# Kernel optimization log

Hardware: AMD Instinct MI355X
Metric: run time of the kernel (lower is better)

## Reference

```python
import jax, jax.numpy as jnp
import numpy as np

B, T, S, F, D, M = 8, 8192, 8192, 64, 64, 128
EPS = 1e-9


def _draw_omega(n_omega, d_feature, rng):
    # Stacked orthogonal blocks scaled by sqrt(d_feature), as in the TF module.
    n_blocks = (n_omega + d_feature - 1) // d_feature + 1
    blocks = []
    for _ in range(n_blocks):
        g = rng.standard_normal((d_feature, d_feature)).astype(np.float32)
        q, _ = np.linalg.qr(g)
        blocks.append(q * np.sqrt(float(d_feature)))
    return jnp.asarray(np.concatenate(blocks, axis=0)[:n_omega])


def setup_inputs() -> dict:
    k0 = jax.random.key(0)
    kq, kv, kk = jax.random.split(k0, 3)
    query = jax.random.normal(kq, (B, T, F), dtype=jnp.float32)
    value = jax.random.normal(kv, (B, S, D), dtype=jnp.float32)
    key = jax.random.normal(kk, (B, S, F), dtype=jnp.float32)
    omega = _draw_omega(M, F, np.random.default_rng(0))  # (M, F)
    return {"query": query, "value": value, "key": key, "omega": omega}


def _phi(x, omega):
    # x: (B, L, F) -> (B, L, 2M) positive random features
    m = omega.shape[0]
    square_sum = jnp.sum(x * x, axis=-1, keepdims=True) / 2.0  # (B, L, 1)
    xw = jnp.einsum('blf,mf->blm', x, omega)                   # (B, L, M)
    unnorm = jnp.exp(jnp.concatenate([xw, -xw], axis=-1) - square_sum) + EPS
    return unnorm / jnp.sqrt(2.0 * m)


def reference(query, value, key, omega):
    q = _phi(query, omega)  # (B, T, 2M)
    k = _phi(key, omega)    # (B, S, 2M)
    ones = jnp.ones(value.shape[:-1] + (1,), dtype=value.dtype)
    v1 = jnp.concatenate([value, ones], axis=-1)               # (B, S, D+1)
    kv = jnp.einsum('bsm,bsd->bmd', k, v1)                     # (B, 2M, D+1)
    qkv = jnp.einsum('btm,bmd->btd', q, kv)                    # (B, T, D+1)
    normalizer = qkv[:, :, -1:]
    return qkv[:, :, :-1] / normalizer
```

## Files before the change

### kernel.cpp

```cpp
#include <hip/hip_runtime.h>


constexpr int NB = 8;
constexpr int NT = 8192;
constexpr float EPSF = 1e-9f;
constexpr float SCALE = 0.0625f;

typedef short s8v __attribute__((ext_vector_type(8)));
typedef short s4v __attribute__((ext_vector_type(4)));
typedef float f4v __attribute__((ext_vector_type(4)));

__device__ inline f4v mfma16(s8v a, s8v b, f4v c) {
  return __builtin_amdgcn_mfma_f32_16x16x32_bf16(a, b, c, 0, 0, 0);
}

__device__ inline short bf16_rne(float f) {
  unsigned u = __builtin_bit_cast(unsigned, f);
  u += 0x7fffu + ((u >> 16) & 1u);
  return (short)(u >> 16);
}
__device__ inline float bf16_to_f(short h) {
  unsigned u = ((unsigned)(unsigned short)h) << 16;
  return __builtin_bit_cast(float, u);
}

__global__ void setup_omega(const float* __restrict__ omega,
                            short* __restrict__ oh, short* __restrict__ ol) {
  int i = blockIdx.x * 256 + threadIdx.x;
  if (i >= 128 * 64) return;
  float w = omega[i];
  short h = bf16_rne(w);
  oh[i] = h;
  ol[i] = bf16_rne(w - bf16_to_f(h));
}

struct PhiRows {
  s8v ah0, al0, ah1, al1;
  float ssr[4];
  float ss;
};

__device__ inline void split8(f4v a, f4v b, s8v& h, s8v& l) {
  float v[8] = {a.x, a.y, a.z, a.w, b.x, b.y, b.z, b.w};
#pragma unroll
  for (int j = 0; j < 8; ++j) {
    short hh = bf16_rne(v[j]);
    h[j] = hh;
    l[j] = bf16_rne(v[j] - bf16_to_f(hh));
  }
}

__device__ inline void load_phi_rows(const float* __restrict__ xrow_base, int lane, PhiRows& P) {
  const int r = lane & 15, q = lane >> 4;
  const float* p = xrow_base + r * 64 + q * 8;
  f4v u0 = *(const f4v*)(p);
  f4v u1 = *(const f4v*)(p + 4);
  f4v u2 = *(const f4v*)(p + 32);
  f4v u3 = *(const f4v*)(p + 36);
  float ss = u0.x * u0.x + u0.y * u0.y + u0.z * u0.z + u0.w * u0.w
           + u1.x * u1.x + u1.y * u1.y + u1.z * u1.z + u1.w * u1.w
           + u2.x * u2.x + u2.y * u2.y + u2.z * u2.z + u2.w * u2.w
           + u3.x * u3.x + u3.y * u3.y + u3.z * u3.z + u3.w * u3.w;
  ss += __shfl_xor(ss, 16, 64);
  ss += __shfl_xor(ss, 32, 64);
  ss *= 0.5f;
  P.ss = ss;
#pragma unroll
  for (int reg = 0; reg < 4; ++reg) P.ssr[reg] = __shfl(ss, q * 4 + reg, 64);
  split8(u0, u1, P.ah0, P.al0);
  split8(u2, u3, P.ah1, P.al1);
}

__device__ inline f4v phi_xw_tile(const PhiRows& P, const short* __restrict__ oh,
                                  const short* __restrict__ ol, int f0, int lane) {
  const int fr = f0 + (lane & 15);
  const int q = lane >> 4;
  s8v bh0 = *(const s8v*)(oh + fr * 64 + q * 8);
  s8v bh1 = *(const s8v*)(oh + fr * 64 + 32 + q * 8);
  s8v bl0 = *(const s8v*)(ol + fr * 64 + q * 8);
  s8v bl1 = *(const s8v*)(ol + fr * 64 + 32 + q * 8);
  f4v c = {0.f, 0.f, 0.f, 0.f};
  c = mfma16(P.ah0, bh0, c);
  c = mfma16(P.ah1, bh1, c);
  c = mfma16(P.al0, bh0, c);
  c = mfma16(P.al1, bh1, c);
  c = mfma16(P.ah0, bl0, c);
  c = mfma16(P.ah1, bl1, c);
  return c;
}

__device__ inline f4v phi_xw_tile_T(const PhiRows& P, const short* __restrict__ oh,
                                    const short* __restrict__ ol, int f0, int lane) {
  const int fr = f0 + (lane & 15);
  const int q = lane >> 4;
  s8v ah0 = *(const s8v*)(oh + fr * 64 + q * 8);
  s8v ah1 = *(const s8v*)(oh + fr * 64 + 32 + q * 8);
  s8v al0 = *(const s8v*)(ol + fr * 64 + q * 8);
  s8v al1 = *(const s8v*)(ol + fr * 64 + 32 + q * 8);
  f4v c = {0.f, 0.f, 0.f, 0.f};
  c = mfma16(ah0, P.ah0, c);
  c = mfma16(ah1, P.ah1, c);
  c = mfma16(al0, P.ah0, c);
  c = mfma16(al1, P.ah1, c);
  c = mfma16(ah0, P.al0, c);
  c = mfma16(ah1, P.al1, c);
  return c;
}

constexpr int KF_P = 72;
constexpr int QF_P = 264;
constexpr int PART_SZ = 65 * 256;

__global__ __launch_bounds__(256, 2) void kv_fused(
    const float* __restrict__ key, const float* __restrict__ value,
    const short* __restrict__ oh, const short* __restrict__ ol,
    short* __restrict__ partial, float* __restrict__ kvacc, int use_partial) {
  __shared__ short kft[256 * KF_P];
  __shared__ short v1t[80 * KF_P];
  const int tid = threadIdx.x, lane = tid & 63, w = tid >> 6;
  const int b = blockIdx.x >> 6;
  const int s0 = (blockIdx.x & 63) * 128;
  const int q = lane >> 4, r15 = lane & 15;

  for (int i = tid; i < 15 * KF_P; i += 256) v1t[65 * KF_P + i] = 0;

  f4v acc[4][5];
#pragma unroll
  for (int j = 0; j < 4; ++j)
#pragma unroll
    for (int n = 0; n < 5; ++n) acc[j][n] = f4v{0.f, 0.f, 0.f, 0.f};

  for (int sc = 0; sc < 2; ++sc) {
    const int sbase = s0 + sc * 64;
    __syncthreads();
    {
      const float* vb = value + ((size_t)b * NT + sbase) * 64;
#pragma unroll
      for (int i = 0; i < 4; ++i) {
        int e4 = tid + i * 256;
        f4v v4 = ((const f4v*)vb)[e4];
        int s = e4 >> 4, d0 = (e4 & 15) * 4;
        v1t[(d0 + 0) * KF_P + s] = bf16_rne(v4.x);
        v1t[(d0 + 1) * KF_P + s] = bf16_rne(v4.y);
        v1t[(d0 + 2) * KF_P + s] = bf16_rne(v4.z);
        v1t[(d0 + 3) * KF_P + s] = bf16_rne(v4.w);
      }
      if (tid < 64) v1t[64 * KF_P + tid] = (short)0x3F80;
    }
    {
      PhiRows P;
      load_phi_rows(key + ((size_t)b * NT + sbase + w * 16) * 64, lane, P);
#pragma unroll
      for (int ft = 0; ft < 8; ++ft) {
        f4v c = phi_xw_tile(P, oh, ol, ft * 16, lane);
        s4v pk, nk;
#pragma unroll
        for (int reg = 0; reg < 4; ++reg) {
          float xw = c[reg];
          pk[reg] = bf16_rne((__expf(xw - P.ssr[reg]) + EPSF) * SCALE);
          nk[reg] = bf16_rne((__expf(-xw - P.ssr[reg]) + EPSF) * SCALE);
        }
        const int scol = w * 16 + q * 4;
        *(s4v*)(kft + (ft * 16 + r15) * KF_P + scol) = pk;
        *(s4v*)(kft + (128 + ft * 16 + r15) * KF_P + scol) = nk;
      }
    }
    __syncthreads();
#pragma unroll
    for (int ks = 0; ks < 2; ++ks) {
      s8v bf[5];
#pragma unroll
      for (int n = 0; n < 5; ++n)
        bf[n] = *(const s8v*)(v1t + (n * 16 + r15) * KF_P + ks * 32 + q * 8);
#pragma unroll
      for (int j = 0; j < 4; ++j) {
        s8v a = *(const s8v*)(kft + (w * 64 + j * 16 + r15) * KF_P + ks * 32 + q * 8);
#pragma unroll
        for (int n = 0; n < 5; ++n) acc[j][n] = mfma16(a, bf[n], acc[j][n]);
      }
    }
  }
  if (use_partial) {
    short* pb = partial + (size_t)blockIdx.x * PART_SZ;
#pragma unroll
    for (int j = 0; j < 4; ++j) {
      int m = w * 64 + j * 16 + q * 4;
#pragma unroll
      for (int n = 0; n < 4; ++n) {
        int d = n * 16 + r15;
        s4v pk;
#pragma unroll
        for (int reg = 0; reg < 4; ++reg) pk[reg] = bf16_rne(acc[j][n][reg]);
        *(s4v*)(pb + d * 256 + m) = pk;
      }
      if (r15 == 0) {
        s4v pk;
#pragma unroll
        for (int reg = 0; reg < 4; ++reg) pk[reg] = bf16_rne(acc[j][4][reg]);
        *(s4v*)(pb + 64 * 256 + m) = pk;
      }
    }
  } else {
    float* pb = kvacc + (size_t)b * PART_SZ;
#pragma unroll
    for (int j = 0; j < 4; ++j) {
      int m = w * 64 + j * 16 + q * 4;
#pragma unroll
      for (int n = 0; n < 4; ++n) {
        int d = n * 16 + r15;
#pragma unroll
        for (int reg = 0; reg < 4; ++reg) atomicAdd(pb + d * 256 + m + reg, acc[j][n][reg]);
      }
      if (r15 == 0)
#pragma unroll
        for (int reg = 0; reg < 4; ++reg) atomicAdd(pb + 64 * 256 + m + reg, acc[j][4][reg]);
    }
  }
}

__global__ __launch_bounds__(256) void kv_finalize(
    const short* __restrict__ partial, const float* __restrict__ kvacc,
    short* __restrict__ kvfrag, int use_partial) {
  int i = blockIdx.x * 256 + threadIdx.x;
  int b = i / 20480;
  int rem = i - b * 20480;
  int d = rem >> 8;
  int m = rem & 255;
  float s = 0.f;
  if (d < 65) {
    if (use_partial) {
      const short* p = partial + (size_t)(b * 64) * PART_SZ + d * 256 + m;
#pragma unroll 8
      for (int c = 0; c < 64; ++c) s += bf16_to_f(p[(size_t)c * PART_SZ]);
    } else {
      s = kvacc[(size_t)b * PART_SZ + d * 256 + m];
    }
  }
  int ks = m >> 5, qq = (m >> 3) & 3, j = m & 7;
  int n = d >> 4, r = d & 15;
  int lane = qq * 16 + r;
  kvfrag[(((size_t)b * 40 + ks * 5 + n) * 64 + lane) * 8 + j] = bf16_rne(s);
}

__global__ __launch_bounds__(256, 4) void qkv_fused(
    const float* __restrict__ query, const short* __restrict__ oh,
    const short* __restrict__ ol, const short* __restrict__ kvfrag,
    float* __restrict__ out) {
  __shared__ __align__(16) short qf[64 * QF_P];
  const int tid = threadIdx.x, lane = tid & 63, w = tid >> 6;
  const int b = blockIdx.x >> 7;
  const int t0 = (blockIdx.x & 127) * 64;
  const int q = lane >> 4, r15 = lane & 15;

  {
    PhiRows P;
    load_phi_rows(query + ((size_t)b * NT + t0 + w * 16) * 64, lane, P);
    const int t_loc = w * 16 + r15;
#pragma unroll
    for (int ft = 0; ft < 8; ++ft) {
      f4v c = phi_xw_tile_T(P, oh, ol, ft * 16, lane);
      s4v pk, nk;
#pragma unroll
      for (int reg = 0; reg < 4; ++reg) {
        float xw = c[reg];
        pk[reg] = bf16_rne((__expf(xw - P.ss) + EPSF) * SCALE);
        nk[reg] = bf16_rne((__expf(-xw - P.ss) + EPSF) * SCALE);
      }
      *(s4v*)(qf + t_loc * QF_P + ft * 16 + q * 4) = pk;
      *(s4v*)(qf + t_loc * QF_P + 128 + ft * 16 + q * 4) = nk;
    }
  }
  f4v acc[5];
#pragma unroll
  for (int n = 0; n < 5; ++n) acc[n] = f4v{0.f, 0.f, 0.f, 0.f};
  const short* kvb = kvfrag + (size_t)b * 40 * 512;
#pragma unroll
  for (int ks = 0; ks < 8; ++ks) {
    s8v a = *(const s8v*)(qf + (w * 16 + r15) * QF_P + ks * 32 + q * 8);
#pragma unroll
    for (int n = 0; n < 5; ++n) {
      s8v bf = *(const s8v*)(kvb + ((size_t)(ks * 5 + n)) * 512 + lane * 8);
      acc[n] = mfma16(a, bf, acc[n]);
    }
  }
  float den_r[4];
#pragma unroll
  for (int reg = 0; reg < 4; ++reg) den_r[reg] = __shfl(acc[4][reg], lane & 48, 64);
  float* stg = (float*)(qf + w * 16 * QF_P);
#pragma unroll
  for (int n = 0; n < 4; ++n)
#pragma unroll
    for (int reg = 0; reg < 4; ++reg) {
      int row = q * 4 + reg;
      int col = n * 16 + r15;
      stg[row * 68 + col] = acc[n][reg] / den_r[reg];
    }
  float* ob = out + ((size_t)b * NT + t0 + w * 16) * 64;
#pragma unroll
  for (int rr = 0; rr < 4; ++rr) {
    int row = rr * 4 + q;
    int c4 = r15 * 4;
    *(f4v*)(ob + row * 64 + c4) = *(const f4v*)(stg + row * 68 + c4);
  }
}

extern "C" void kernel_launch(void* const* d_in, const int* in_sizes, int n_in,
                              void* d_out, int out_size, void* d_ws, size_t ws_size,
                              hipStream_t stream) {
  const float* query = (const float*)d_in[0];
  const float* value = (const float*)d_in[1];
  const float* key   = (const float*)d_in[2];
  const float* omega = (const float*)d_in[3];
  float* out = (float*)d_out;

  char* ws = (char*)d_ws;
  short* oh = (short*)ws;
  short* ol = (short*)(ws + 16384);
  short* kvfrag = (short*)(ws + 32768);
  short* partial = (short*)(ws + 360448);
  float* kvacc = (float*)(ws + 360448);
  const size_t need_full = 360448 + (size_t)512 * PART_SZ * 2;
  const int use_partial = (ws_size >= need_full) ? 1 : 0;

  setup_omega<<<32, 256, 0, stream>>>(omega, oh, ol);
  if (!use_partial) {
    hipMemsetAsync(kvacc, 0, (size_t)8 * PART_SZ * 4, stream);
  }
  kv_fused<<<512, 256, 0, stream>>>(key, value, oh, ol, partial, kvacc, use_partial);
  kv_finalize<<<640, 256, 0, stream>>>(partial, kvacc, kvfrag, use_partial);
  qkv_fused<<<1024, 256, 0, stream>>>(query, oh, ol, kvfrag, out);
}
```

Measured before the change: 142.6 us.

## Make kv_fused waves independent and pre-swizzle omega into MFMA fragment order

Omega hi/lo bf16 splits are now stored in MFMA fragment order, so each lane reads contiguous 16-byte chunks. In kv_fused, each wave now computes its own slice of phi(key): one sign (positive or negative) and half of the feature columns, over all 64 keys of the chunk. It writes that slice to a private LDS region, which removes both __syncthreads per chunk. The value tile is no longer staged through LDS; each lane loads it straight from global memory with strided scalar reads and converts to bf16, and the ones column is built in registers. The cost is redundant key loads and phi setup across waves, plus uncoalesced global reads of value.

```diff
diff --git a/kernel.cpp b/kernel.cpp
--- a/kernel.cpp
+++ b/kernel.cpp
@@ -25,13 +25,19 @@
 }
 
 __global__ void setup_omega(const float* __restrict__ omega,
-                            short* __restrict__ oh, short* __restrict__ ol) {
+                            short* __restrict__ ohf, short* __restrict__ olf) {
   int i = blockIdx.x * 256 + threadIdx.x;
   if (i >= 128 * 64) return;
-  float w = omega[i];
-  short h = bf16_rne(w);
-  oh[i] = h;
-  ol[i] = bf16_rne(w - bf16_to_f(h));
+  int jj = i & 7;
+  int lane = (i >> 3) & 63;
+  int h = (i >> 9) & 1;
+  int ft = i >> 10;
+  int m = ft * 16 + (lane & 15);
+  int f = h * 32 + (lane >> 4) * 8 + jj;
+  float wv = omega[m * 64 + f];
+  short hh = bf16_rne(wv);
+  ohf[i] = hh;
+  olf[i] = bf16_rne(wv - bf16_to_f(hh));
 }
 
 struct PhiRows {
@@ -71,14 +77,13 @@
   split8(u2, u3, P.ah1, P.al1);
 }
 
-__device__ inline f4v phi_xw_tile(const PhiRows& P, const short* __restrict__ oh,
-                                  const short* __restrict__ ol, int f0, int lane) {
-  const int fr = f0 + (lane & 15);
-  const int q = lane >> 4;
-  s8v bh0 = *(const s8v*)(oh + fr * 64 + q * 8);
-  s8v bh1 = *(const s8v*)(oh + fr * 64 + 32 + q * 8);
-  s8v bl0 = *(const s8v*)(ol + fr * 64 + q * 8);
-  s8v bl1 = *(const s8v*)(ol + fr * 64 + 32 + q * 8);
+__device__ inline f4v phi_xw_tile(const PhiRows& P, const short* __restrict__ ohf,
+                                  const short* __restrict__ olf, int ft, int lane) {
+  const int o0 = ft * 1024 + lane * 8;
+  s8v bh0 = *(const s8v*)(ohf + o0);
+  s8v bh1 = *(const s8v*)(ohf + o0 + 512);
+  s8v bl0 = *(const s8v*)(olf + o0);
+  s8v bl1 = *(const s8v*)(olf + o0 + 512);
   f4v c = {0.f, 0.f, 0.f, 0.f};
   c = mfma16(P.ah0, bh0, c);
   c = mfma16(P.ah1, bh1, c);
@@ -89,14 +94,13 @@
   return c;
 }
 
-__device__ inline f4v phi_xw_tile_T(const PhiRows& P, const short* __restrict__ oh,
-                                    const short* __restrict__ ol, int f0, int lane) {
-  const int fr = f0 + (lane & 15);
-  const int q = lane >> 4;
-  s8v ah0 = *(const s8v*)(oh + fr * 64 + q * 8);
-  s8v ah1 = *(const s8v*)(oh + fr * 64 + 32 + q * 8);
-  s8v al0 = *(const s8v*)(ol + fr * 64 + q * 8);
-  s8v al1 = *(const s8v*)(ol + fr * 64 + 32 + q * 8);
+__device__ inline f4v phi_xw_tile_T(const PhiRows& P, const short* __restrict__ ohf,
+                                    const short* __restrict__ olf, int ft, int lane) {
+  const int o0 = ft * 1024 + lane * 8;
+  s8v ah0 = *(const s8v*)(ohf + o0);
+  s8v ah1 = *(const s8v*)(ohf + o0 + 512);
+  s8v al0 = *(const s8v*)(olf + o0);
+  s8v al1 = *(const s8v*)(olf + o0 + 512);
   f4v c = {0.f, 0.f, 0.f, 0.f};
   c = mfma16(ah0, P.ah0, c);
   c = mfma16(ah1, P.ah1, c);
@@ -113,16 +117,19 @@
 
 __global__ __launch_bounds__(256, 2) void kv_fused(
     const float* __restrict__ key, const float* __restrict__ value,
-    const short* __restrict__ oh, const short* __restrict__ ol,
+    const short* __restrict__ ohf, const short* __restrict__ olf,
     short* __restrict__ partial, float* __restrict__ kvacc, int use_partial) {
-  __shared__ short kft[256 * KF_P];
-  __shared__ short v1t[80 * KF_P];
+  __shared__ short kft[4 * 64 * KF_P];
   const int tid = threadIdx.x, lane = tid & 63, w = tid >> 6;
   const int b = blockIdx.x >> 6;
   const int s0 = (blockIdx.x & 63) * 128;
   const int q = lane >> 4, r15 = lane & 15;
-
-  for (int i = tid; i < 15 * KF_P; i += 256) v1t[65 * KF_P + i] = 0;
+  const int sign = w >> 1, th = w & 1;
+  short* kw = kft + w * 64 * KF_P;
+
+  s8v vone;
+#pragma unroll
+  for (int jj = 0; jj < 8; ++jj) vone[jj] = (r15 == 0) ? (short)0x3F80 : (short)0;
 
   f4v acc[4][5];
 #pragma unroll
@@ -132,49 +139,37 @@
 
   for (int sc = 0; sc < 2; ++sc) {
     const int sbase = s0 + sc * 64;
-    __syncthreads();
-    {
-      const float* vb = value + ((size_t)b * NT + sbase) * 64;
-#pragma unroll
-      for (int i = 0; i < 4; ++i) {
-        int e4 = tid + i * 256;
-        f4v v4 = ((const f4v*)vb)[e4];
-        int s = e4 >> 4, d0 = (e4 & 15) * 4;
-        v1t[(d0 + 0) * KF_P + s] = bf16_rne(v4.x);
-        v1t[(d0 + 1) * KF_P + s] = bf16_rne(v4.y);
-        v1t[(d0 + 2) * KF_P + s] = bf16_rne(v4.z);
-        v1t[(d0 + 3) * KF_P + s] = bf16_rne(v4.w);
-      }
-      if (tid < 64) v1t[64 * KF_P + tid] = (short)0x3F80;
-    }
-    {
+#pragma unroll
+    for (int rg = 0; rg < 4; ++rg) {
       PhiRows P;
-      load_phi_rows(key + ((size_t)b * NT + sbase + w * 16) * 64, lane, P);
-#pragma unroll
-      for (int ft = 0; ft < 8; ++ft) {
-        f4v c = phi_xw_tile(P, oh, ol, ft * 16, lane);
-        s4v pk, nk;
+      load_phi_rows(key + ((size_t)b * NT + sbase + rg * 16) * 64, lane, P);
+#pragma unroll
+      for (int j = 0; j < 4; ++j) {
+        f4v c = phi_xw_tile(P, ohf, olf, th * 4 + j, lane);
+        s4v pk;
 #pragma unroll
         for (int reg = 0; reg < 4; ++reg) {
           float xw = c[reg];
-          pk[reg] = bf16_rne((__expf(xw - P.ssr[reg]) + EPSF) * SCALE);
-          nk[reg] = bf16_rne((__expf(-xw - P.ssr[reg]) + EPSF) * SCALE);
+          float arg = sign ? (-xw - P.ssr[reg]) : (xw - P.ssr[reg]);
+          pk[reg] = bf16_rne((__expf(arg) + EPSF) * SCALE);
         }
-        const int scol = w * 16 + q * 4;
-        *(s4v*)(kft + (ft * 16 + r15) * KF_P + scol) = pk;
-        *(s4v*)(kft + (128 + ft * 16 + r15) * KF_P + scol) = nk;
-      }
-    }
-    __syncthreads();
+        *(s4v*)(kw + (j * 16 + r15) * KF_P + rg * 16 + q * 4) = pk;
+      }
+    }
+    const float* vb = value + ((size_t)b * NT + sbase) * 64;
 #pragma unroll
     for (int ks = 0; ks < 2; ++ks) {
       s8v bf[5];
 #pragma unroll
-      for (int n = 0; n < 5; ++n)
-        bf[n] = *(const s8v*)(v1t + (n * 16 + r15) * KF_P + ks * 32 + q * 8);
+      for (int n = 0; n < 4; ++n) {
+#pragma unroll
+        for (int jj = 0; jj < 8; ++jj)
+          bf[n][jj] = bf16_rne(vb[(ks * 32 + q * 8 + jj) * 64 + n * 16 + r15]);
+      }
+      bf[4] = vone;
 #pragma unroll
       for (int j = 0; j < 4; ++j) {
-        s8v a = *(const s8v*)(kft + (w * 64 + j * 16 + r15) * KF_P + ks * 32 + q * 8);
+        s8v a = *(const s8v*)(kw + (j * 16 + r15) * KF_P + ks * 32 + q * 8);
 #pragma unroll
         for (int n = 0; n < 5; ++n) acc[j][n] = mfma16(a, bf[n], acc[j][n]);
       }
@@ -243,8 +238,8 @@
 }
 
 __global__ __launch_bounds__(256, 4) void qkv_fused(
-    const float* __restrict__ query, const short* __restrict__ oh,
-    const short* __restrict__ ol, const short* __restrict__ kvfrag,
+    const float* __restrict__ query, const short* __restrict__ ohf,
+    const short* __restrict__ olf, const short* __restrict__ kvfrag,
     float* __restrict__ out) {
   __shared__ __align__(16) short qf[64 * QF_P];
   const int tid = threadIdx.x, lane = tid & 63, w = tid >> 6;
@@ -258,7 +253,7 @@
     const int t_loc = w * 16 + r15;
 #pragma unroll
     for (int ft = 0; ft < 8; ++ft) {
-      f4v c = phi_xw_tile_T(P, oh, ol, ft * 16, lane);
+      f4v c = phi_xw_tile_T(P, ohf, olf, ft, lane);
       s4v pk, nk;
 #pragma unroll
       for (int reg = 0; reg < 4; ++reg) {
@@ -314,19 +309,19 @@
   float* out = (float*)d_out;
 
   char* ws = (char*)d_ws;
-  short* oh = (short*)ws;
-  short* ol = (short*)(ws + 16384);
+  short* ohf = (short*)ws;
+  short* olf = (short*)(ws + 16384);
   short* kvfrag = (short*)(ws + 32768);
   short* partial = (short*)(ws + 360448);
   float* kvacc = (float*)(ws + 360448);
   const size_t need_full = 360448 + (size_t)512 * PART_SZ * 2;
   const int use_partial = (ws_size >= need_full) ? 1 : 0;
 
-  setup_omega<<<32, 256, 0, stream>>>(omega, oh, ol);
+  setup_omega<<<32, 256, 0, stream>>>(omega, ohf, olf);
   if (!use_partial) {
     hipMemsetAsync(kvacc, 0, (size_t)8 * PART_SZ * 4, stream);
   }
-  kv_fused<<<512, 256, 0, stream>>>(key, value, oh, ol, partial, kvacc, use_partial);
+  kv_fused<<<512, 256, 0, stream>>>(key, value, ohf, olf, partial, kvacc, use_partial);
   kv_finalize<<<640, 256, 0, stream>>>(partial, kvacc, kvfrag, use_partial);
-  qkv_fused<<<1024, 256, 0, stream>>>(query, oh, ol, kvfrag, out);
-}
+  qkv_fused<<<1024, 256, 0, stream>>>(query, ohf, olf, kvfrag, out);
+}
```

New measurement: 131.4 us. -7.8%, faster.
